# Kernel tuning notes

Hardware: AMD Instinct MI355X
Metric: run time of the kernel (lower is better)

The kernel has to match this reference:

```python
import jax, jax.numpy as jnp
import numpy as np

N, E = 100000, 1600000
IN_C, HID = 64, 128
HID2 = HID // 2


def _sage_conv(x, edge_index, W_l, b_l, W_r):
    # PyG SAGEConv (mean aggr): out = lin_l(mean_{j in N(i)} x_j) + lin_r(x_i)
    src, dst = edge_index[0], edge_index[1]
    n = x.shape[0]
    msgs = x[src]  # [E, d] gather of source node features
    agg_sum = jax.ops.segment_sum(msgs, dst, num_segments=n)  # [N, d]
    deg = jax.ops.segment_sum(jnp.ones((msgs.shape[0],), x.dtype), dst, num_segments=n)
    agg = agg_sum / jnp.maximum(deg, 1.0)[:, None]  # mean; 0 for isolated nodes
    return agg @ W_l + b_l + x @ W_r


def setup_inputs() -> dict:
    key = jax.random.key(0)
    ks = jax.random.split(key, 10)
    s = lambda fan_in: 1.0 / np.sqrt(fan_in)
    return {
        "x": jax.random.normal(ks[0], (N, IN_C), jnp.float32),
        "edge_index": jax.random.randint(ks[1], (2, E), 0, N, jnp.int64),
        "W1_l": jax.random.uniform(ks[2], (IN_C, HID), jnp.float32, -s(IN_C), s(IN_C)),
        "b1": jnp.zeros((HID,), jnp.float32),
        "W1_r": jax.random.uniform(ks[3], (IN_C, HID), jnp.float32, -s(IN_C), s(IN_C)),
        "W2_l": jax.random.uniform(ks[4], (HID, HID2), jnp.float32, -s(HID), s(HID)),
        "b2": jnp.zeros((HID2,), jnp.float32),
        "W2_r": jax.random.uniform(ks[5], (HID, HID2), jnp.float32, -s(HID), s(HID)),
        "Wfc": jax.random.uniform(ks[6], (HID2, 1), jnp.float32, -s(HID2), s(HID2)),
        "bfc": jnp.zeros((1,), jnp.float32),
    }


def reference(x, edge_index, W1_l, b1, W1_r, W2_l, b2, W2_r, Wfc, bfc):
    h = jax.nn.relu(_sage_conv(x, edge_index, W1_l, b1, W1_r))
    # dropout p=0.3 is identity at inference (training=False)
    h = jax.nn.relu(_sage_conv(h, edge_index, W2_l, b2, W2_r))
    return jax.nn.sigmoid(h @ Wfc + bfc)
```

## Files before the change

kernel.cpp:

```cpp
#include <hip/hip_runtime.h>
#include <hip/hip_bf16.h>
#include <math.h>


#define IN_C 64
#define HID 128
#define HID2 64
#define LDA 136
#define NBSHIFT 9
#define BR 512
#define P1B 256

typedef short short8 __attribute__((ext_vector_type(8)));
typedef float f32x4 __attribute__((ext_vector_type(4)));
typedef float f32x2 __attribute__((ext_vector_type(2)));

__device__ inline unsigned short bfbits(float f) {
    __hip_bfloat16 h = __float2bfloat16(f);
    return *reinterpret_cast<unsigned short*>(&h);
}
__device__ inline float bflo(unsigned u) { return __uint_as_float(u << 16); }
__device__ inline float bfhi(unsigned u) { return __uint_as_float(u & 0xffff0000u); }
__device__ inline unsigned bfpack(float a, float b) {
    return ((unsigned)bfbits(b) << 16) | (unsigned)bfbits(a);
}
__device__ inline unsigned char f_to_fp8(float v) {
    return (unsigned char)(__builtin_amdgcn_cvt_pk_fp8_f32(v, v, 0, false) & 0xff);
}
__device__ inline void accum16(uint4 u, float* acc) {
    f32x2 p;
    p = __builtin_amdgcn_cvt_pk_f32_fp8((int)u.x, false); acc[0] += p[0];  acc[1] += p[1];
    p = __builtin_amdgcn_cvt_pk_f32_fp8((int)u.x, true);  acc[2] += p[0];  acc[3] += p[1];
    p = __builtin_amdgcn_cvt_pk_f32_fp8((int)u.y, false); acc[4] += p[0];  acc[5] += p[1];
    p = __builtin_amdgcn_cvt_pk_f32_fp8((int)u.y, true);  acc[6] += p[0];  acc[7] += p[1];
    p = __builtin_amdgcn_cvt_pk_f32_fp8((int)u.z, false); acc[8] += p[0];  acc[9] += p[1];
    p = __builtin_amdgcn_cvt_pk_f32_fp8((int)u.z, true);  acc[10] += p[0]; acc[11] += p[1];
    p = __builtin_amdgcn_cvt_pk_f32_fp8((int)u.w, false); acc[12] += p[0]; acc[13] += p[1];
    p = __builtin_amdgcn_cvt_pk_f32_fp8((int)u.w, true);  acc[14] += p[0]; acc[15] += p[1];
}

#define AGG_LOOP(TBL)                                                       \
    const uint4* tbl = TBL;                                                 \
    int itmax = (m + 7) >> 3;                                               \
    int ecur = s0 + jl;                                                     \
    int hi = s1 - 1;                                                        \
    int src_a = __builtin_nontemporal_load(&srcs[max(min(ecur, hi), 0)]);   \
    int src_b = __builtin_nontemporal_load(&srcs[max(min(ecur + 4, hi), 0)]);\
    for (int it = 0; it < itmax; ++it) {                                    \
        int enx = ecur + 8;                                                 \
        int na = 0, nb = 0;                                                 \
        if (it + 1 < itmax) {                                               \
            na = __builtin_nontemporal_load(&srcs[max(min(enx, hi), 0)]);   \
            nb = __builtin_nontemporal_load(&srcs[max(min(enx + 4, hi), 0)]);\
        }                                                                   \
        int sa0 = __builtin_amdgcn_ds_swizzle(src_a, 0x1C);                 \
        int sa1 = __builtin_amdgcn_ds_swizzle(src_a, 0x3C);                 \
        int sa2 = __builtin_amdgcn_ds_swizzle(src_a, 0x5C);                 \
        int sa3 = __builtin_amdgcn_ds_swizzle(src_a, 0x7C);                 \
        int sb0 = __builtin_amdgcn_ds_swizzle(src_b, 0x1C);                 \
        int sb1 = __builtin_amdgcn_ds_swizzle(src_b, 0x3C);                 \
        int sb2 = __builtin_amdgcn_ds_swizzle(src_b, 0x5C);                 \
        int sb3 = __builtin_amdgcn_ds_swizzle(src_b, 0x7C);                 \
        uint4 u0 = tbl[(unsigned)(sa0 * 4 + jl)];                           \
        uint4 u1 = tbl[(unsigned)(sa1 * 4 + jl)];                           \
        uint4 u2 = tbl[(unsigned)(sa2 * 4 + jl)];                           \
        uint4 u3 = tbl[(unsigned)(sa3 * 4 + jl)];                           \
        uint4 u4 = tbl[(unsigned)(sb0 * 4 + jl)];                           \
        uint4 u5 = tbl[(unsigned)(sb1 * 4 + jl)];                           \
        uint4 u6 = tbl[(unsigned)(sb2 * 4 + jl)];                           \
        uint4 u7 = tbl[(unsigned)(sb3 * 4 + jl)];                           \
        int K = it * 8;                                                     \
        if (K + 0 < deg) accum16(u0, acc);                                  \
        if (K + 1 < deg) accum16(u1, acc);                                  \
        if (K + 2 < deg) accum16(u2, acc);                                  \
        if (K + 3 < deg) accum16(u3, acc);                                  \
        if (K + 4 < deg) accum16(u4, acc);                                  \
        if (K + 5 < deg) accum16(u5, acc);                                  \
        if (K + 6 < deg) accum16(u6, acc);                                  \
        if (K + 7 < deg) accum16(u7, acc);                                  \
        src_a = na; src_b = nb; ecur = enx;                                 \
    }

__global__ __launch_bounds__(256) void count_kernel(
    const int* __restrict__ ei, int* __restrict__ cnt,
    const float4* __restrict__ x4, unsigned* __restrict__ xf8,
    int* __restrict__ histg, int* __restrict__ gcnt2,
    const float* __restrict__ W1l, const float* __restrict__ W1r,
    const float* __restrict__ W2l, const float* __restrict__ W2r,
    unsigned short* __restrict__ Wb1, unsigned short* __restrict__ Wb2,
    int n4, int E, int EPB, int NBUCK)
{
    __shared__ int hist[256];
    int t = threadIdx.x, j = blockIdx.x;
    hist[t] = 0;
    if (j == 0) { histg[t] = 0; gcnt2[t] = 0; }
    if (j < 16) {
        int tw = j * 256 + t;
        for (int i = tw; i < 16384; i += 4096) {
            int n = i & 127, k = i >> 7;
            float v = (k < 64) ? W1l[k * HID + n] : W1r[(k - 64) * HID + n];
            Wb1[n * 128 + k] = bfbits(v);
        }
        for (int i = tw; i < 16384; i += 4096) {
            int n = i & 127, c = i >> 7;
            float v = (n < 64) ? W2l[c * HID2 + n] : W2r[c * HID2 + (n - 64)];
            Wb2[n * 128 + c] = bfbits(v);
        }
    }
    __syncthreads();
    int e0 = j * EPB, e1 = min(e0 + EPB, E);
    for (int e = e0 + t; e < e1; e += 256)
        atomicAdd(&hist[ei[E + e] >> NBSHIFT], 1);
    for (int i = j * 256 + t; i < n4; i += P1B * 256) {
        float4 f = x4[i];
        int lo = __builtin_amdgcn_cvt_pk_fp8_f32(f.x, f.y, 0, false);
        xf8[i] = (unsigned)__builtin_amdgcn_cvt_pk_fp8_f32(f.z, f.w, lo, true);
    }
    __syncthreads();
    if (t < NBUCK) cnt[j * NBUCK + t] = hist[t];
}

__global__ __launch_bounds__(256) void scatter_kernel(
    const int* __restrict__ ei, const int* __restrict__ cnt,
    int* __restrict__ bucket_base, int* __restrict__ row_ptr,
    int* __restrict__ part, int N, int E, int EPB, int NBUCK)
{
    __shared__ int tot[256];
    __shared__ int lofs[256];
    __shared__ int wred[4];
    int t = threadIdx.x, j = blockIdx.x;
    int lane = t & 63, w = t >> 6;
    int pre = 0, total = 0;
    if (t < NBUCK) {
        for (int jj = 0; jj < P1B; ++jj) {
            int c = cnt[jj * NBUCK + t];
            total += c;
            if (jj < j) pre += c;
        }
    }
    tot[t] = (t < NBUCK) ? total : 0;
    __syncthreads();
    int v = tot[t];
    int x = v;
    for (int off = 1; off < 64; off <<= 1) {
        int u = __shfl_up(x, off);
        if (lane >= off) x += u;
    }
    if (lane == 63) wred[w] = x;
    __syncthreads();
    int add = 0;
    for (int k = 0; k < w; ++k) add += wred[k];
    int bb = x + add - v;
    lofs[t] = bb + pre;
    if (j == 0) {
        if (t < NBUCK) bucket_base[t] = bb;
        if (t == 0) { bucket_base[NBUCK] = E; row_ptr[N] = E; }
    }
    __syncthreads();
    int e0 = j * EPB, e1 = min(e0 + EPB, E);
    for (int e = e0 + t; e < e1; e += 256) {
        int s = ei[e], d = ei[E + e];
        int b = d >> NBSHIFT;
        int p = atomicAdd(&lofs[b], 1);
        part[p] = (s << NBSHIFT) | (d & (BR - 1));
    }
}

__global__ __launch_bounds__(256) void csr_kernel(
    const int* __restrict__ part, const int* __restrict__ bucket_base,
    int* __restrict__ row_ptr, int* __restrict__ srcs,
    int* __restrict__ histg, int N)
{
    __shared__ int ncnt[BR];
    __shared__ int nofs[BR];
    __shared__ int nfill[BR];
    __shared__ int wred[4];
    __shared__ int dh[256];
    int b = blockIdx.x;
    int t = threadIdx.x, lane = t & 63, w = t >> 6;
    int node0 = b << NBSHIFT;
    int nn = min(BR, N - node0);
    int gb0 = bucket_base[b], gb1 = bucket_base[b + 1];
    ncnt[t] = 0; ncnt[t + 256] = 0; dh[t] = 0;
    __syncthreads();
    for (int i = gb0 + t; i < gb1; i += 256)
        atomicAdd(&ncnt[part[i] & (BR - 1)], 1);
    __syncthreads();
    for (int i = t; i < nn; i += 256)
        atomicAdd(&dh[min(ncnt[i], 255)], 1);
    int c0 = ncnt[2 * t], c1 = ncnt[2 * t + 1];
    int v = c0 + c1;
    int x = v;
    for (int off = 1; off < 64; off <<= 1) {
        int u = __shfl_up(x, off);
        if (lane >= off) x += u;
    }
    if (lane == 63) wred[w] = x;
    __syncthreads();
    int add = 0;
    for (int k = 0; k < w; ++k) add += wred[k];
    int exc = x + add - v;
    nofs[2 * t] = exc;          nofs[2 * t + 1] = exc + c0;
    nfill[2 * t] = exc;         nfill[2 * t + 1] = exc + c0;
    __syncthreads();
    if (dh[t]) atomicAdd(&histg[t], dh[t]);
    for (int i = t; i < nn; i += 256) row_ptr[node0 + i] = gb0 + nofs[i];
    for (int i = gb0 + t; i < gb1; i += 256) {
        int p = part[i];
        int pos = atomicAdd(&nfill[p & (BR - 1)], 1);
        srcs[gb0 + pos] = ((unsigned)p) >> NBSHIFT;
    }
}

__global__ __launch_bounds__(256) void dsort_kernel(
    const int* __restrict__ row_ptr, const int* __restrict__ histg,
    int* __restrict__ gcnt2, int* __restrict__ dsorted, int N)
{
    __shared__ int base[256];
    __shared__ int wred[4];
    __shared__ int lcnt[256];
    __shared__ int bbase[256];
    int t = threadIdx.x, lane = t & 63, w = t >> 6;
    int v = histg[t];
    int x = v;
    for (int off = 1; off < 64; off <<= 1) {
        int u = __shfl_up(x, off);
        if (lane >= off) x += u;
    }
    if (lane == 63) wred[w] = x;
    lcnt[t] = 0;
    __syncthreads();
    int add = 0;
    for (int k = 0; k < w; ++k) add += wred[k];
    base[t] = x + add - v;
    __syncthreads();
    int n = blockIdx.x * 256 + t;
    int bin = 0, lr = 0;
    if (n < N) {
        int deg = row_ptr[n + 1] - row_ptr[n];
        bin = min(deg, 255);
        lr = atomicAdd(&lcnt[bin], 1);
    }
    __syncthreads();
    if (lcnt[t] > 0) bbase[t] = atomicAdd(&gcnt2[t], lcnt[t]);
    __syncthreads();
    if (n < N) dsorted[base[bin] + bbase[bin] + lr] = n;
}

__global__ __launch_bounds__(256) void agg1_kernel(
    const uint4* __restrict__ xf8q, const int* __restrict__ row_ptr,
    const int* __restrict__ srcs, const int* __restrict__ dsorted,
    unsigned* __restrict__ M1u, int N)
{
    int t = threadIdx.x;
    int lane = t & 63, wv = t >> 6;
    int slot = blockIdx.x * 64 + wv * 16 + (lane >> 2);
    int jl = lane & 3;
    bool live = slot < N;
    int node = dsorted[live ? slot : 0];
    int s0 = row_ptr[node], s1 = row_ptr[node + 1];
    int deg = live ? (s1 - s0) : 0;
    int m = deg;
    m = max(m, __shfl_xor(m, 4));  m = max(m, __shfl_xor(m, 8));
    m = max(m, __shfl_xor(m, 16)); m = max(m, __shfl_xor(m, 32));

    float acc[16];
#pragma unroll
    for (int i = 0; i < 16; ++i) acc[i] = 0.f;

    AGG_LOOP(xf8q)

    float scale = deg > 0 ? 1.f / (float)deg : 0.f;
    if (live) {
        uint4 o0, o1;
        o0.x = bfpack(acc[0] * scale, acc[1] * scale);
        o0.y = bfpack(acc[2] * scale, acc[3] * scale);
        o0.z = bfpack(acc[4] * scale, acc[5] * scale);
        o0.w = bfpack(acc[6] * scale, acc[7] * scale);
        o1.x = bfpack(acc[8] * scale, acc[9] * scale);
        o1.y = bfpack(acc[10] * scale, acc[11] * scale);
        o1.z = bfpack(acc[12] * scale, acc[13] * scale);
        o1.w = bfpack(acc[14] * scale, acc[15] * scale);
        uint4* dst = (uint4*)(M1u + (size_t)node * 32) + jl * 2;
        dst[0] = o0; dst[1] = o1;
    }
}

__global__ __launch_bounds__(256) void dense_kernel(
    const unsigned short* __restrict__ M1s, const float* __restrict__ x,
    const unsigned short* __restrict__ Wb1, const float* __restrict__ b1,
    const unsigned short* __restrict__ Wb2, unsigned* __restrict__ G8,
    unsigned* __restrict__ S2u, int N)
{
    __shared__ unsigned short sA[64 * LDA];
    __shared__ unsigned short sB[128 * LDA];
    int tid = threadIdx.x;
    int base = blockIdx.x * 64;

    const uint4* wb1q = (const uint4*)Wb1;
    for (int i = tid; i < 2048; i += 256) {
        int n = i >> 4, s = i & 15;
        *(uint4*)&sB[n * LDA + s * 8] = wb1q[i];
    }
    const uint4* m1q = (const uint4*)M1s;
    const float4* xq = (const float4*)x;
    for (int i = tid; i < 512; i += 256) {
        int r = i >> 3, s = i & 7;
        int node = min(base + r, N - 1);
        *(uint4*)&sA[r * LDA + s * 8] = m1q[(size_t)node * 8 + s];
    }
    for (int i = tid; i < 512; i += 256) {
        int r = i >> 3, s = i & 7;
        int node = min(base + r, N - 1);
        float4 f0 = xq[(size_t)node * 16 + s * 2];
        float4 f1 = xq[(size_t)node * 16 + s * 2 + 1];
        uint4 u;
        u.x = bfpack(f0.x, f0.y); u.y = bfpack(f0.z, f0.w);
        u.z = bfpack(f1.x, f1.y); u.w = bfpack(f1.z, f1.w);
        *(uint4*)&sA[r * LDA + 64 + s * 8] = u;
    }
    __syncthreads();

    int w = tid >> 6, lane = tid & 63;
    int m0 = w * 16;
    int mr = lane & 15, q = lane >> 4;
    const f32x4 zero = {0.f, 0.f, 0.f, 0.f};

    f32x4 acc[8];
#pragma unroll
    for (int nt = 0; nt < 8; ++nt) acc[nt] = zero;

#pragma unroll
    for (int kt = 0; kt < 4; ++kt) {
        short8 a0 = *reinterpret_cast<const short8*>(&sA[(m0 + mr) * LDA + kt * 32 + q * 8]);
#pragma unroll
        for (int nt = 0; nt < 8; ++nt) {
            short8 b = *reinterpret_cast<const short8*>(&sB[(nt * 16 + mr) * LDA + kt * 32 + q * 8]);
            acc[nt] = __builtin_amdgcn_mfma_f32_16x16x32_bf16(a0, b, acc[nt], 0, 0, 0);
        }
    }
    __syncthreads();

#pragma unroll
    for (int nt = 0; nt < 8; ++nt)
#pragma unroll
        for (int j = 0; j < 4; ++j) {
            int row = m0 + q * 4 + j;
            int col = nt * 16 + mr;
            float v = acc[nt][j] + b1[col];
            sA[row * LDA + col] = bfbits(fmaxf(v, 0.f));
        }
    const uint4* wb2q = (const uint4*)Wb2;
    for (int i = tid; i < 2048; i += 256) {
        int n = i >> 4, s = i & 15;
        *(uint4*)&sB[n * LDA + s * 8] = wb2q[i];
    }
    __syncthreads();

    f32x4 acc2[8];
#pragma unroll
    for (int nt = 0; nt < 8; ++nt) acc2[nt] = zero;

#pragma unroll
    for (int kt = 0; kt < 4; ++kt) {
        short8 a0 = *reinterpret_cast<const short8*>(&sA[(m0 + mr) * LDA + kt * 32 + q * 8]);
#pragma unroll
        for (int nt = 0; nt < 8; ++nt) {
            short8 b = *reinterpret_cast<const short8*>(&sB[(nt * 16 + mr) * LDA + kt * 32 + q * 8]);
            acc2[nt] = __builtin_amdgcn_mfma_f32_16x16x32_bf16(a0, b, acc2[nt], 0, 0, 0);
        }
    }
    __syncthreads();

    unsigned char* sG = (unsigned char*)sA;
    unsigned short* sS = (unsigned short*)sB;
#pragma unroll
    for (int nt = 0; nt < 8; ++nt)
#pragma unroll
        for (int j = 0; j < 4; ++j) {
            int row = m0 + q * 4 + j;
            int col = nt * 16 + mr;
            float v = acc2[nt][j];
            if (col < 64) sG[row * 64 + col] = f_to_fp8(v);
            else          sS[row * 64 + (col - 64)] = bfbits(v);
        }
    __syncthreads();
    const unsigned* sGu = (const unsigned*)sG;
    for (int i = tid; i < 64 * 16; i += 256) {
        int r = i >> 4, node = base + r;
        if (node < N) G8[(size_t)node * 16 + (i & 15)] = sGu[i];
    }
    const unsigned* sSu = (const unsigned*)sS;
    for (int i = tid; i < 64 * 32; i += 256) {
        int r = i >> 5, node = base + r;
        if (node < N) S2u[(size_t)node * 32 + (i & 31)] = sSu[i];
    }
}

__global__ __launch_bounds__(256) void agg2fc_kernel(
    const uint4* __restrict__ G8q, const int* __restrict__ row_ptr,
    const int* __restrict__ srcs, const int* __restrict__ dsorted,
    const unsigned* __restrict__ S2u, const float* __restrict__ b2,
    const float* __restrict__ Wfc, const float* __restrict__ bfc,
    float* __restrict__ out, int N)
{
    int t = threadIdx.x;
    int lane = t & 63, wv = t >> 6;
    int slot = blockIdx.x * 64 + wv * 16 + (lane >> 2);
    int jl = lane & 3;
    bool live = slot < N;
    int node = dsorted[live ? slot : 0];
    int s0 = row_ptr[node], s1 = row_ptr[node + 1];
    int deg = live ? (s1 - s0) : 0;
    int m = deg;
    m = max(m, __shfl_xor(m, 4));  m = max(m, __shfl_xor(m, 8));
    m = max(m, __shfl_xor(m, 16)); m = max(m, __shfl_xor(m, 32));

    const uint4* s2p = (const uint4*)(S2u + (size_t)node * 32) + jl * 2;
    uint4 sa = s2p[0], sb = s2p[1];

    float acc[16];
#pragma unroll
    for (int i = 0; i < 16; ++i) acc[i] = 0.f;

    AGG_LOOP(G8q)

    float scale = deg > 0 ? 1.f / (float)deg : 0.f;
    float z = 0.f;
    if (live) {
        const float4* b4p = ((const float4*)b2) + jl * 4;
        const float4* w4p = ((const float4*)Wfc) + jl * 4;
        unsigned sw0 = sa.x, sw1 = sa.y, sw2 = sa.z, sw3 = sa.w;
        unsigned sw4 = sb.x, sw5 = sb.y, sw6 = sb.z, sw7 = sb.w;
        float4 b4, w4;
        b4 = b4p[0]; w4 = w4p[0];
        z += fmaxf(acc[0]  * scale + bflo(sw0) + b4.x, 0.f) * w4.x;
        z += fmaxf(acc[1]  * scale + bfhi(sw0) + b4.y, 0.f) * w4.y;
        z += fmaxf(acc[2]  * scale + bflo(sw1) + b4.z, 0.f) * w4.z;
        z += fmaxf(acc[3]  * scale + bfhi(sw1) + b4.w, 0.f) * w4.w;
        b4 = b4p[1]; w4 = w4p[1];
        z += fmaxf(acc[4]  * scale + bflo(sw2) + b4.x, 0.f) * w4.x;
        z += fmaxf(acc[5]  * scale + bfhi(sw2) + b4.y, 0.f) * w4.y;
        z += fmaxf(acc[6]  * scale + bflo(sw3) + b4.z, 0.f) * w4.z;
        z += fmaxf(acc[7]  * scale + bfhi(sw3) + b4.w, 0.f) * w4.w;
        b4 = b4p[2]; w4 = w4p[2];
        z += fmaxf(acc[8]  * scale + bflo(sw4) + b4.x, 0.f) * w4.x;
        z += fmaxf(acc[9]  * scale + bfhi(sw4) + b4.y, 0.f) * w4.y;
        z += fmaxf(acc[10] * scale + bflo(sw5) + b4.z, 0.f) * w4.z;
        z += fmaxf(acc[11] * scale + bfhi(sw5) + b4.w, 0.f) * w4.w;
        b4 = b4p[3]; w4 = w4p[3];
        z += fmaxf(acc[12] * scale + bflo(sw6) + b4.x, 0.f) * w4.x;
        z += fmaxf(acc[13] * scale + bfhi(sw6) + b4.y, 0.f) * w4.y;
        z += fmaxf(acc[14] * scale + bflo(sw7) + b4.z, 0.f) * w4.z;
        z += fmaxf(acc[15] * scale + bfhi(sw7) + b4.w, 0.f) * w4.w;
    }
    z += __shfl_xor(z, 1); z += __shfl_xor(z, 2);
    if (live && jl == 0) out[node] = 1.f / (1.f + __expf(-(z + bfc[0])));
}

static inline size_t align_up(size_t v, size_t a) { return (v + a - 1) & ~(a - 1); }

extern "C" void kernel_launch(void* const* d_in, const int* in_sizes, int n_in,
                              void* d_out, int out_size, void* d_ws, size_t ws_size,
                              hipStream_t stream) {
    const float* x   = (const float*)d_in[0];
    const int*   ei  = (const int*)d_in[1];
    const float* W1l = (const float*)d_in[2];
    const float* b1  = (const float*)d_in[3];
    const float* W1r = (const float*)d_in[4];
    const float* W2l = (const float*)d_in[5];
    const float* b2  = (const float*)d_in[6];
    const float* W2r = (const float*)d_in[7];
    const float* Wfc = (const float*)d_in[8];
    const float* bfc = (const float*)d_in[9];
    float* out = (float*)d_out;

    const int N = in_sizes[0] / IN_C;
    const int E = in_sizes[1] / 2;
    const int NBUCK = (N + BR - 1) / BR;
    const int EPB = (E + P1B - 1) / P1B;

    char* ws = (char*)d_ws;
    size_t o = 0;
    int* row_ptr  = (int*)(ws + o); o = align_up(o + (size_t)(N + 1) * 4, 256);
    int* srcs     = (int*)(ws + o); o = align_up(o + (size_t)E * 4, 256);
    int* cnt      = (int*)(ws + o); o = align_up(o + (size_t)P1B * 256 * 4, 256);
    int* bb       = (int*)(ws + o); o = align_up(o + 257 * 4, 256);
    int* histg    = (int*)(ws + o); o = align_up(o + 256 * 4, 256);
    int* gcnt2    = (int*)(ws + o); o = align_up(o + 256 * 4, 256);
    int* dsorted  = (int*)(ws + o); o = align_up(o + (size_t)N * 4, 256);
    unsigned short* Wb1 = (unsigned short*)(ws + o); o = align_up(o + 16384 * 2, 256);
    unsigned short* Wb2 = (unsigned short*)(ws + o); o = align_up(o + 16384 * 2, 256);
    size_t part_off = o;
    size_t sz1 = (size_t)E * 4, sz2 = (size_t)N * 128;
    o = align_up(part_off + (sz1 > sz2 ? sz1 : sz2), 256);
    int* part = (int*)(ws + part_off);
    unsigned* S2u = (unsigned*)(ws + part_off);
    unsigned* xf8 = (unsigned*)(ws + o); o = align_up(o + (size_t)N * 16 * 4, 256);
    unsigned* M1u = (unsigned*)(ws + o); o = align_up(o + (size_t)N * 32 * 4, 256);
    unsigned* G8  = (unsigned*)(ws + o); o = align_up(o + (size_t)N * 16 * 4, 256);

    count_kernel<<<P1B, 256, 0, stream>>>(ei, cnt, (const float4*)x, xf8,
                                          histg, gcnt2, W1l, W1r, W2l, W2r,
                                          Wb1, Wb2, N * 16, E, EPB, NBUCK);
    scatter_kernel<<<P1B, 256, 0, stream>>>(ei, cnt, bb, row_ptr, part,
                                            N, E, EPB, NBUCK);
    csr_kernel<<<NBUCK, 256, 0, stream>>>(part, bb, row_ptr, srcs, histg, N);
    dsort_kernel<<<(N + 255) / 256, 256, 0, stream>>>(row_ptr, histg, gcnt2,
                                                      dsorted, N);

    int gab = (N + 63) / 64;
    agg1_kernel<<<gab, 256, 0, stream>>>((const uint4*)xf8, row_ptr, srcs,
                                         dsorted, M1u, N);
    dense_kernel<<<(N + 63) / 64, 256, 0, stream>>>(
        (const unsigned short*)M1u, x, Wb1, b1, Wb2, G8, S2u, N);
    agg2fc_kernel<<<gab, 256, 0, stream>>>((const uint4*)G8, row_ptr, srcs,
                                           dsorted, S2u, b2, Wfc, bfc, out, N);
}
```

Baseline: 235.5 us.

## Split fp8 feature tables into two halves and aggregate each in a separate pass

The 64-channel fp8 node feature tables (x and layer-2 G) are split into two 32-byte halves stored in separate arrays, and each aggregation kernel runs twice, once per half. Each pass gathers 8-byte rows from a half-size table, which may fit better in L2/MALL and cut random-gather traffic misses, and it halves the accumulator registers. In exchange, the edge list and row pointers are read twice, there are two extra launches, and the final sigmoid relies on the second pass reading the partial sum written to out by the first.

```diff
diff --git a/kernel.cpp b/kernel.cpp
--- a/kernel.cpp
+++ b/kernel.cpp
@@ -27,20 +27,16 @@
 __device__ inline unsigned char f_to_fp8(float v) {
     return (unsigned char)(__builtin_amdgcn_cvt_pk_fp8_f32(v, v, 0, false) & 0xff);
 }
-__device__ inline void accum16(uint4 u, float* acc) {
+__device__ inline void accum8(uint2 u, float* acc) {
     f32x2 p;
-    p = __builtin_amdgcn_cvt_pk_f32_fp8((int)u.x, false); acc[0] += p[0];  acc[1] += p[1];
-    p = __builtin_amdgcn_cvt_pk_f32_fp8((int)u.x, true);  acc[2] += p[0];  acc[3] += p[1];
-    p = __builtin_amdgcn_cvt_pk_f32_fp8((int)u.y, false); acc[4] += p[0];  acc[5] += p[1];
-    p = __builtin_amdgcn_cvt_pk_f32_fp8((int)u.y, true);  acc[6] += p[0];  acc[7] += p[1];
-    p = __builtin_amdgcn_cvt_pk_f32_fp8((int)u.z, false); acc[8] += p[0];  acc[9] += p[1];
-    p = __builtin_amdgcn_cvt_pk_f32_fp8((int)u.z, true);  acc[10] += p[0]; acc[11] += p[1];
-    p = __builtin_amdgcn_cvt_pk_f32_fp8((int)u.w, false); acc[12] += p[0]; acc[13] += p[1];
-    p = __builtin_amdgcn_cvt_pk_f32_fp8((int)u.w, true);  acc[14] += p[0]; acc[15] += p[1];
-}
-
-#define AGG_LOOP(TBL)                                                       \
-    const uint4* tbl = TBL;                                                 \
+    p = __builtin_amdgcn_cvt_pk_f32_fp8((int)u.x, false); acc[0] += p[0]; acc[1] += p[1];
+    p = __builtin_amdgcn_cvt_pk_f32_fp8((int)u.x, true);  acc[2] += p[0]; acc[3] += p[1];
+    p = __builtin_amdgcn_cvt_pk_f32_fp8((int)u.y, false); acc[4] += p[0]; acc[5] += p[1];
+    p = __builtin_amdgcn_cvt_pk_f32_fp8((int)u.y, true);  acc[6] += p[0]; acc[7] += p[1];
+}
+
+#define AGG_LOOP_U2(TBL)                                                    \
+    const uint2* tbl = TBL;                                                 \
     int itmax = (m + 7) >> 3;                                               \
     int ecur = s0 + jl;                                                     \
     int hi = s1 - 1;                                                        \
@@ -61,30 +57,31 @@
         int sb1 = __builtin_amdgcn_ds_swizzle(src_b, 0x3C);                 \
         int sb2 = __builtin_amdgcn_ds_swizzle(src_b, 0x5C);                 \
         int sb3 = __builtin_amdgcn_ds_swizzle(src_b, 0x7C);                 \
-        uint4 u0 = tbl[(unsigned)(sa0 * 4 + jl)];                           \
-        uint4 u1 = tbl[(unsigned)(sa1 * 4 + jl)];                           \
-        uint4 u2 = tbl[(unsigned)(sa2 * 4 + jl)];                           \
-        uint4 u3 = tbl[(unsigned)(sa3 * 4 + jl)];                           \
-        uint4 u4 = tbl[(unsigned)(sb0 * 4 + jl)];                           \
-        uint4 u5 = tbl[(unsigned)(sb1 * 4 + jl)];                           \
-        uint4 u6 = tbl[(unsigned)(sb2 * 4 + jl)];                           \
-        uint4 u7 = tbl[(unsigned)(sb3 * 4 + jl)];                           \
+        uint2 u0 = tbl[(unsigned)(sa0 * 4 + jl)];                           \
+        uint2 u1 = tbl[(unsigned)(sa1 * 4 + jl)];                           \
+        uint2 u2 = tbl[(unsigned)(sa2 * 4 + jl)];                           \
+        uint2 u3 = tbl[(unsigned)(sa3 * 4 + jl)];                           \
+        uint2 u4 = tbl[(unsigned)(sb0 * 4 + jl)];                           \
+        uint2 u5 = tbl[(unsigned)(sb1 * 4 + jl)];                           \
+        uint2 u6 = tbl[(unsigned)(sb2 * 4 + jl)];                           \
+        uint2 u7 = tbl[(unsigned)(sb3 * 4 + jl)];                           \
         int K = it * 8;                                                     \
-        if (K + 0 < deg) accum16(u0, acc);                                  \
-        if (K + 1 < deg) accum16(u1, acc);                                  \
-        if (K + 2 < deg) accum16(u2, acc);                                  \
-        if (K + 3 < deg) accum16(u3, acc);                                  \
-        if (K + 4 < deg) accum16(u4, acc);                                  \
-        if (K + 5 < deg) accum16(u5, acc);                                  \
-        if (K + 6 < deg) accum16(u6, acc);                                  \
-        if (K + 7 < deg) accum16(u7, acc);                                  \
+        if (K + 0 < deg) accum8(u0, acc);                                   \
+        if (K + 1 < deg) accum8(u1, acc);                                   \
+        if (K + 2 < deg) accum8(u2, acc);                                   \
+        if (K + 3 < deg) accum8(u3, acc);                                   \
+        if (K + 4 < deg) accum8(u4, acc);                                   \
+        if (K + 5 < deg) accum8(u5, acc);                                   \
+        if (K + 6 < deg) accum8(u6, acc);                                   \
+        if (K + 7 < deg) accum8(u7, acc);                                   \
         src_a = na; src_b = nb; ecur = enx;                                 \
     }
 
 __global__ __launch_bounds__(256) void count_kernel(
     const int* __restrict__ ei, int* __restrict__ cnt,
-    const float4* __restrict__ x4, unsigned* __restrict__ xf8,
-    int* __restrict__ histg, int* __restrict__ gcnt2,
+    const float4* __restrict__ x4, unsigned* __restrict__ xf8a,
+    unsigned* __restrict__ xf8b, int* __restrict__ histg,
+    int* __restrict__ gcnt2,
     const float* __restrict__ W1l, const float* __restrict__ W1r,
     const float* __restrict__ W2l, const float* __restrict__ W2r,
     unsigned short* __restrict__ Wb1, unsigned short* __restrict__ Wb2,
@@ -114,7 +111,11 @@
     for (int i = j * 256 + t; i < n4; i += P1B * 256) {
         float4 f = x4[i];
         int lo = __builtin_amdgcn_cvt_pk_fp8_f32(f.x, f.y, 0, false);
-        xf8[i] = (unsigned)__builtin_amdgcn_cvt_pk_fp8_f32(f.z, f.w, lo, true);
+        unsigned v = (unsigned)__builtin_amdgcn_cvt_pk_fp8_f32(f.z, f.w, lo, true);
+        int node = i >> 4, w2 = i & 15;
+        unsigned* dst = (w2 < 8) ? (xf8a + (size_t)node * 8 + w2)
+                                 : (xf8b + (size_t)node * 8 + (w2 - 8));
+        *dst = v;
     }
     __syncthreads();
     if (t < NBUCK) cnt[j * NBUCK + t] = hist[t];
@@ -248,9 +249,9 @@
 }
 
 __global__ __launch_bounds__(256) void agg1_kernel(
-    const uint4* __restrict__ xf8q, const int* __restrict__ row_ptr,
+    const uint2* __restrict__ H, const int* __restrict__ row_ptr,
     const int* __restrict__ srcs, const int* __restrict__ dsorted,
-    unsigned* __restrict__ M1u, int N)
+    unsigned* __restrict__ M1u, int N, int half)
 {
     int t = threadIdx.x;
     int lane = t & 63, wv = t >> 6;
@@ -264,33 +265,28 @@
     m = max(m, __shfl_xor(m, 4));  m = max(m, __shfl_xor(m, 8));
     m = max(m, __shfl_xor(m, 16)); m = max(m, __shfl_xor(m, 32));
 
-    float acc[16];
-#pragma unroll
-    for (int i = 0; i < 16; ++i) acc[i] = 0.f;
-
-    AGG_LOOP(xf8q)
+    float acc[8];
+#pragma unroll
+    for (int i = 0; i < 8; ++i) acc[i] = 0.f;
+
+    AGG_LOOP_U2(H)
 
     float scale = deg > 0 ? 1.f / (float)deg : 0.f;
     if (live) {
-        uint4 o0, o1;
-        o0.x = bfpack(acc[0] * scale, acc[1] * scale);
-        o0.y = bfpack(acc[2] * scale, acc[3] * scale);
-        o0.z = bfpack(acc[4] * scale, acc[5] * scale);
-        o0.w = bfpack(acc[6] * scale, acc[7] * scale);
-        o1.x = bfpack(acc[8] * scale, acc[9] * scale);
-        o1.y = bfpack(acc[10] * scale, acc[11] * scale);
-        o1.z = bfpack(acc[12] * scale, acc[13] * scale);
-        o1.w = bfpack(acc[14] * scale, acc[15] * scale);
-        uint4* dst = (uint4*)(M1u + (size_t)node * 32) + jl * 2;
-        dst[0] = o0; dst[1] = o1;
+        uint4 o;
+        o.x = bfpack(acc[0] * scale, acc[1] * scale);
+        o.y = bfpack(acc[2] * scale, acc[3] * scale);
+        o.z = bfpack(acc[4] * scale, acc[5] * scale);
+        o.w = bfpack(acc[6] * scale, acc[7] * scale);
+        ((uint4*)(M1u + (size_t)node * 32))[half * 4 + jl] = o;
     }
 }
 
 __global__ __launch_bounds__(256) void dense_kernel(
     const unsigned short* __restrict__ M1s, const float* __restrict__ x,
     const unsigned short* __restrict__ Wb1, const float* __restrict__ b1,
-    const unsigned short* __restrict__ Wb2, unsigned* __restrict__ G8,
-    unsigned* __restrict__ S2u, int N)
+    const unsigned short* __restrict__ Wb2, unsigned* __restrict__ G8a,
+    unsigned* __restrict__ G8b, unsigned* __restrict__ S2u, int N)
 {
     __shared__ unsigned short sA[64 * LDA];
     __shared__ unsigned short sB[128 * LDA];
@@ -387,8 +383,11 @@
     __syncthreads();
     const unsigned* sGu = (const unsigned*)sG;
     for (int i = tid; i < 64 * 16; i += 256) {
-        int r = i >> 4, node = base + r;
-        if (node < N) G8[(size_t)node * 16 + (i & 15)] = sGu[i];
+        int r = i >> 4, node = base + r, wd = i & 15;
+        if (node < N) {
+            if (wd < 8) G8a[(size_t)node * 8 + wd] = sGu[i];
+            else        G8b[(size_t)node * 8 + (wd - 8)] = sGu[i];
+        }
     }
     const unsigned* sSu = (const unsigned*)sS;
     for (int i = tid; i < 64 * 32; i += 256) {
@@ -398,11 +397,11 @@
 }
 
 __global__ __launch_bounds__(256) void agg2fc_kernel(
-    const uint4* __restrict__ G8q, const int* __restrict__ row_ptr,
+    const uint2* __restrict__ H, const int* __restrict__ row_ptr,
     const int* __restrict__ srcs, const int* __restrict__ dsorted,
     const unsigned* __restrict__ S2u, const float* __restrict__ b2,
     const float* __restrict__ Wfc, const float* __restrict__ bfc,
-    float* __restrict__ out, int N)
+    float* __restrict__ out, int N, int half)
 {
     int t = threadIdx.x;
     int lane = t & 63, wv = t >> 6;
@@ -416,46 +415,37 @@
     m = max(m, __shfl_xor(m, 4));  m = max(m, __shfl_xor(m, 8));
     m = max(m, __shfl_xor(m, 16)); m = max(m, __shfl_xor(m, 32));
 
-    const uint4* s2p = (const uint4*)(S2u + (size_t)node * 32) + jl * 2;
-    uint4 sa = s2p[0], sb = s2p[1];
-
-    float acc[16];
-#pragma unroll
-    for (int i = 0; i < 16; ++i) acc[i] = 0.f;
-
-    AGG_LOOP(G8q)
+    uint4 sa = ((const uint4*)(S2u + (size_t)node * 32))[half * 4 + jl];
+
+    float acc[8];
+#pragma unroll
+    for (int i = 0; i < 8; ++i) acc[i] = 0.f;
+
+    AGG_LOOP_U2(H)
 
     float scale = deg > 0 ? 1.f / (float)deg : 0.f;
     float z = 0.f;
     if (live) {
-        const float4* b4p = ((const float4*)b2) + jl * 4;
-        const float4* w4p = ((const float4*)Wfc) + jl * 4;
+        const float4* b4p = ((const float4*)b2) + half * 8 + jl * 2;
+        const float4* w4p = ((const float4*)Wfc) + half * 8 + jl * 2;
         unsigned sw0 = sa.x, sw1 = sa.y, sw2 = sa.z, sw3 = sa.w;
-        unsigned sw4 = sb.x, sw5 = sb.y, sw6 = sb.z, sw7 = sb.w;
         float4 b4, w4;
         b4 = b4p[0]; w4 = w4p[0];
-        z += fmaxf(acc[0]  * scale + bflo(sw0) + b4.x, 0.f) * w4.x;
-        z += fmaxf(acc[1]  * scale + bfhi(sw0) + b4.y, 0.f) * w4.y;
-        z += fmaxf(acc[2]  * scale + bflo(sw1) + b4.z, 0.f) * w4.z;
-        z += fmaxf(acc[3]  * scale + bfhi(sw1) + b4.w, 0.f) * w4.w;
+        z += fmaxf(acc[0] * scale + bflo(sw0) + b4.x, 0.f) * w4.x;
+        z += fmaxf(acc[1] * scale + bfhi(sw0) + b4.y, 0.f) * w4.y;
+        z += fmaxf(acc[2] * scale + bflo(sw1) + b4.z, 0.f) * w4.z;
+        z += fmaxf(acc[3] * scale + bfhi(sw1) + b4.w, 0.f) * w4.w;
         b4 = b4p[1]; w4 = w4p[1];
-        z += fmaxf(acc[4]  * scale + bflo(sw2) + b4.x, 0.f) * w4.x;
-        z += fmaxf(acc[5]  * scale + bfhi(sw2) + b4.y, 0.f) * w4.y;
-        z += fmaxf(acc[6]  * scale + bflo(sw3) + b4.z, 0.f) * w4.z;
-        z += fmaxf(acc[7]  * scale + bfhi(sw3) + b4.w, 0.f) * w4.w;
-        b4 = b4p[2]; w4 = w4p[2];
-        z += fmaxf(acc[8]  * scale + bflo(sw4) + b4.x, 0.f) * w4.x;
-        z += fmaxf(acc[9]  * scale + bfhi(sw4) + b4.y, 0.f) * w4.y;
-        z += fmaxf(acc[10] * scale + bflo(sw5) + b4.z, 0.f) * w4.z;
-        z += fmaxf(acc[11] * scale + bfhi(sw5) + b4.w, 0.f) * w4.w;
-        b4 = b4p[3]; w4 = w4p[3];
-        z += fmaxf(acc[12] * scale + bflo(sw6) + b4.x, 0.f) * w4.x;
-        z += fmaxf(acc[13] * scale + bfhi(sw6) + b4.y, 0.f) * w4.y;
-        z += fmaxf(acc[14] * scale + bflo(sw7) + b4.z, 0.f) * w4.z;
-        z += fmaxf(acc[15] * scale + bfhi(sw7) + b4.w, 0.f) * w4.w;
+        z += fmaxf(acc[4] * scale + bflo(sw2) + b4.x, 0.f) * w4.x;
+        z += fmaxf(acc[5] * scale + bfhi(sw2) + b4.y, 0.f) * w4.y;
+        z += fmaxf(acc[6] * scale + bflo(sw3) + b4.z, 0.f) * w4.z;
+        z += fmaxf(acc[7] * scale + bfhi(sw3) + b4.w, 0.f) * w4.w;
     }
     z += __shfl_xor(z, 1); z += __shfl_xor(z, 2);
-    if (live && jl == 0) out[node] = 1.f / (1.f + __expf(-(z + bfc[0])));
+    if (live && jl == 0) {
+        if (half == 0) out[node] = z;
+        else out[node] = 1.f / (1.f + __expf(-(z + out[node] + bfc[0])));
+    }
 }
 
 static inline size_t align_up(size_t v, size_t a) { return (v + a - 1) & ~(a - 1); }
@@ -496,11 +486,13 @@
     o = align_up(part_off + (sz1 > sz2 ? sz1 : sz2), 256);
     int* part = (int*)(ws + part_off);
     unsigned* S2u = (unsigned*)(ws + part_off);
-    unsigned* xf8 = (unsigned*)(ws + o); o = align_up(o + (size_t)N * 16 * 4, 256);
-    unsigned* M1u = (unsigned*)(ws + o); o = align_up(o + (size_t)N * 32 * 4, 256);
-    unsigned* G8  = (unsigned*)(ws + o); o = align_up(o + (size_t)N * 16 * 4, 256);
-
-    count_kernel<<<P1B, 256, 0, stream>>>(ei, cnt, (const float4*)x, xf8,
+    unsigned* xf8a = (unsigned*)(ws + o); o = align_up(o + (size_t)N * 32, 256);
+    unsigned* xf8b = (unsigned*)(ws + o); o = align_up(o + (size_t)N * 32, 256);
+    unsigned* M1u  = (unsigned*)(ws + o); o = align_up(o + (size_t)N * 128, 256);
+    unsigned* G8a  = (unsigned*)(ws + o); o = align_up(o + (size_t)N * 32, 256);
+    unsigned* G8b  = (unsigned*)(ws + o); o = align_up(o + (size_t)N * 32, 256);
+
+    count_kernel<<<P1B, 256, 0, stream>>>(ei, cnt, (const float4*)x, xf8a, xf8b,
                                           histg, gcnt2, W1l, W1r, W2l, W2r,
                                           Wb1, Wb2, N * 16, E, EPB, NBUCK);
     scatter_kernel<<<P1B, 256, 0, stream>>>(ei, cnt, bb, row_ptr, part,
@@ -510,10 +502,14 @@
                                                       dsorted, N);
 
     int gab = (N + 63) / 64;
-    agg1_kernel<<<gab, 256, 0, stream>>>((const uint4*)xf8, row_ptr, srcs,
-                                         dsorted, M1u, N);
+    agg1_kernel<<<gab, 256, 0, stream>>>((const uint2*)xf8a, row_ptr, srcs,
+                                         dsorted, M1u, N, 0);
+    agg1_kernel<<<gab, 256, 0, stream>>>((const uint2*)xf8b, row_ptr, srcs,
+                                         dsorted, M1u, N, 1);
     dense_kernel<<<(N + 63) / 64, 256, 0, stream>>>(
-        (const unsigned short*)M1u, x, Wb1, b1, Wb2, G8, S2u, N);
-    agg2fc_kernel<<<gab, 256, 0, stream>>>((const uint4*)G8, row_ptr, srcs,
-                                           dsorted, S2u, b2, Wfc, bfc, out, N);
-}
+        (const unsigned short*)M1u, x, Wb1, b1, Wb2, G8a, G8b, S2u, N);
+    agg2fc_kernel<<<gab, 256, 0, stream>>>((const uint2*)G8a, row_ptr, srcs,
+                                           dsorted, S2u, b2, Wfc, bfc, out, N, 0);
+    agg2fc_kernel<<<gab, 256, 0, stream>>>((const uint2*)G8b, row_ptr, srcs,
+                                           dsorted, S2u, b2, Wfc, bfc, out, N, 1);
+}
```

New measurement: 273.6 us. +16.2%, slower.
